# Optimization experiments

Hardware: AMD Instinct MI355X
Metric: run time of the kernel (lower is better)

Reference implementation:

```python
import jax, jax.numpy as jnp
import numpy as np

HIDDEN = 1024
HEADS = 16
HEAD_DIM = HIDDEN // HEADS
LN_EPS = 1e-6


def setup_inputs() -> dict:
    key = jax.random.key(0)
    ks = jax.random.split(key, 12)
    B, S, H = 2, 2048, HIDDEN
    s = 1.0 / np.sqrt(H)
    inp = {
        "hidden_states": jax.random.normal(ks[0], (B, S, H), dtype=jnp.float32),
        "attention_mask": jnp.ones((B, S), dtype=jnp.int32),
        "Wq": jax.random.normal(ks[1], (H, H), dtype=jnp.float32) * s,
        "bq": jax.random.normal(ks[2], (H,), dtype=jnp.float32) * 0.02,
        "Wk": jax.random.normal(ks[3], (H, H), dtype=jnp.float32) * s,
        "bk": jax.random.normal(ks[4], (H,), dtype=jnp.float32) * 0.02,
        "Wv": jax.random.normal(ks[5], (H, H), dtype=jnp.float32) * s,
        "bv": jax.random.normal(ks[6], (H,), dtype=jnp.float32) * 0.02,
        "Wo": jax.random.normal(ks[7], (H, H), dtype=jnp.float32) * s,
        "bo": jax.random.normal(ks[8], (H,), dtype=jnp.float32) * 0.02,
        "ln_g": jnp.ones((H,), dtype=jnp.float32),
        "ln_b": jnp.zeros((H,), dtype=jnp.float32),
    }
    return inp


def _split_heads(x):
    B, S, H = x.shape
    return x.reshape(B, S, HEADS, HEAD_DIM).transpose(0, 2, 1, 3)  # [B,h,S,d]


def reference(hidden_states, attention_mask, Wq, bq, Wk, bk, Wv, bv, Wo, bo, ln_g, ln_b):
    # torch nn.Linear: y = x @ W.T + b
    q = _split_heads(hidden_states @ Wq.T + bq)
    k = _split_heads(hidden_states @ Wk.T + bk)
    v = _split_heads(hidden_states @ Wv.T + bv)

    scores = jnp.einsum("bhqd,bhkd->bhqk", q, k) / np.sqrt(HEAD_DIM)
    # 2D mask path: [B,K] -> [B,1,1,K]; (1-mask)*-1e18 additive bias
    bias = (1.0 - attention_mask[:, None, None, :].astype(scores.dtype)) * -1e18
    probs = jax.nn.softmax(scores + bias, axis=-1)
    # dropout is identity in eval mode
    ctx = jnp.einsum("bhqk,bhkd->bhqd", probs, v)
    B, h, S, d = ctx.shape
    ctx = ctx.transpose(0, 2, 1, 3).reshape(B, S, h * d)

    out = ctx @ Wo.T + bo
    res = out + hidden_states
    mu = jnp.mean(res, axis=-1, keepdims=True)
    var = jnp.mean(jnp.square(res - mu), axis=-1, keepdims=True)
    return (res - mu) * jax.lax.rsqrt(var + LN_EPS) * ln_g + ln_b
```

## Files before the change

kernel.cpp:

```cpp
#include <hip/hip_runtime.h>
#include <hip/hip_bf16.h>

#define SEQ     2048
#define BATCH   2
#define HID     1024
#define NHEADS  16
#define HD      64
#define MTOT    4096
#define LNEPS   1e-6f
#define L2E     1.4426950408889634f
#define SHIFT2  26.0f

typedef __bf16 bf16_t;
typedef bf16_t bf16x8 __attribute__((ext_vector_type(8)));
typedef bf16_t bf16x4 __attribute__((ext_vector_type(4)));
typedef short  short4v __attribute__((ext_vector_type(4)));
typedef float  floatx4 __attribute__((ext_vector_type(4)));

__device__ __forceinline__ floatx4 mfma16(bf16x8 a, bf16x8 b, floatx4 c) {
    return __builtin_amdgcn_mfma_f32_16x16x32_bf16(a, b, c, 0, 0, 0);
}
__device__ __forceinline__ floatx4 mfma16k16(bf16x4 a, bf16x4 b, floatx4 c) {
    short4v as = __builtin_bit_cast(short4v, a);
    short4v bs = __builtin_bit_cast(short4v, b);
    return __builtin_amdgcn_mfma_f32_16x16x16bf16_1k(as, bs, c, 0, 0, 0);
}
__device__ __forceinline__ bf16x8 ldg8(const bf16_t* p) { return *(const bf16x8*)p; }

__device__ __forceinline__ void stage128x32(const bf16_t* __restrict__ g, int row_stride,
                                            int k0, bf16_t* lds, int wave, int lane)
{
#pragma unroll
    for (int j = 0; j < 2; j++) {
        const int rbase = wave * 32 + j * 16;
        const bf16_t* src = g + (size_t)(rbase + (lane >> 2)) * row_stride + k0 + (lane & 3) * 8;
        bf16_t* dst = lds + rbase * 32;
        __builtin_amdgcn_global_load_lds(
            (const __attribute__((address_space(1))) unsigned int*)src,
            (__attribute__((address_space(3))) unsigned int*)dst, 16, 0, 0);
    }
}
__device__ __forceinline__ void stage64x32(const bf16_t* __restrict__ g, int row_stride,
                                           int k0, bf16_t* lds, int wave, int lane)
{
    const int rbase = wave * 16;
    const bf16_t* src = g + (size_t)(rbase + (lane >> 2)) * row_stride + k0 + (lane & 3) * 8;
    bf16_t* dst = lds + rbase * 32;
    __builtin_amdgcn_global_load_lds(
        (const __attribute__((address_space(1))) unsigned int*)src,
        (__attribute__((address_space(3))) unsigned int*)dst, 16, 0, 0);
}

__global__ __launch_bounds__(256) void cvt_kernel(
    const float* sX, const float* sWq, const float* sWk, const float* sWv, const float* sWo,
    bf16_t* dX, bf16_t* dWq, bf16_t* dWk, bf16_t* dWv, bf16_t* dWo)
{
    const int z = blockIdx.z;
    const float* src; bf16_t* dst; int n;
    switch (z) {
        case 0:  src = sX;  dst = dX;  n = MTOT * HID; break;
        case 1:  src = sWq; dst = dWq; n = HID * HID;  break;
        case 2:  src = sWk; dst = dWk; n = HID * HID;  break;
        case 3:  src = sWv; dst = dWv; n = HID * HID;  break;
        default: src = sWo; dst = dWo; n = HID * HID;  break;
    }
    const int n4 = n >> 2;
    const int stride = gridDim.x * blockDim.x;
    for (int i = blockIdx.x * blockDim.x + threadIdx.x; i < n4; i += stride) {
        const float4 v = ((const float4*)src)[i];
        bf16_t o[4] = {(bf16_t)v.x, (bf16_t)v.y, (bf16_t)v.z, (bf16_t)v.w};
        *(unsigned long long*)(dst + 4 * i) = *(unsigned long long*)o;
    }
}

__global__ __launch_bounds__(256) void qkv_kernel(
    const bf16_t* __restrict__ X,
    const bf16_t* __restrict__ Wq, const float* __restrict__ bq,
    const bf16_t* __restrict__ Wk, const float* __restrict__ bk,
    const bf16_t* __restrict__ Wv, const float* __restrict__ bv,
    bf16_t* __restrict__ Qo, bf16_t* __restrict__ Ko, bf16_t* __restrict__ Vo)
{
    const int z = blockIdx.z;
    const bf16_t* W    = (z == 0) ? Wq : (z == 1) ? Wk : Wv;
    const float*  bias = (z == 0) ? bq : (z == 1) ? bk : bv;
    bf16_t*       out  = (z == 0) ? Qo : (z == 1) ? Ko : Vo;

    const int tid  = threadIdx.x;
    const int lane = tid & 63;
    const int wave = tid >> 6;
    const int l16  = lane & 15;
    const int quad = lane >> 4;
    const int m_blk = blockIdx.y * 128;
    const int n_blk = blockIdx.x * 128;
    const int m_w = (wave >> 1) * 64;
    const int n_w = (wave & 1) * 64;

    __shared__ __align__(16) char smem[18432];
    bf16_t* As = (bf16_t*)smem;
    bf16_t* Bs = (bf16_t*)(smem + 8192);

    floatx4 acc[4][4];
#pragma unroll
    for (int i = 0; i < 4; i++)
#pragma unroll
        for (int j = 0; j < 4; j++) acc[i][j] = (floatx4)0.0f;

    for (int k0 = 0; k0 < HID; k0 += 32) {
        __syncthreads();
        stage128x32(X + (size_t)m_blk * HID, HID, k0, As, wave, lane);
        stage128x32(W + (size_t)n_blk * HID, HID, k0, Bs, wave, lane);
        __syncthreads();

        bf16x8 a[4], b[4];
#pragma unroll
        for (int i = 0; i < 4; i++) a[i] = *(const bf16x8*)&As[(m_w + i * 16 + l16) * 32 + quad * 8];
#pragma unroll
        for (int j = 0; j < 4; j++) b[j] = *(const bf16x8*)&Bs[(n_w + j * 16 + l16) * 32 + quad * 8];
#pragma unroll
        for (int i = 0; i < 4; i++)
#pragma unroll
            for (int j = 0; j < 4; j++) acc[i][j] = mfma16(a[i], b[j], acc[i][j]);
    }
    __syncthreads();

    float bv_[4];
#pragma unroll
    for (int j = 0; j < 4; j++) bv_[j] = bias[n_blk + n_w + j * 16 + l16];

    bf16_t* Tw = (bf16_t*)(smem + wave * 4608);

    if (z != 2) {
        const float scale = (z == 0) ? 0.125f : 1.0f;
        const int hN = (n_blk + n_w) >> 6;
#pragma unroll
        for (int ih = 0; ih < 2; ih++) {
#pragma unroll
            for (int i2 = 0; i2 < 2; i2++) {
                const int i = ih * 2 + i2;
#pragma unroll
                for (int j = 0; j < 4; j++)
#pragma unroll
                    for (int r = 0; r < 4; r++)
                        Tw[(i2 * 16 + quad * 4 + r) * 72 + j * 16 + l16] =
                            (bf16_t)((acc[i][j][r] + bv_[j]) * scale);
            }
#pragma unroll
            for (int p = 0; p < 4; p++) {
                const int srow = p * 8 + (lane >> 3);
                const int col  = (lane & 7) * 8;
                bf16x8 v = *(const bf16x8*)&Tw[srow * 72 + col];
                const int m = m_blk + m_w + ih * 32 + srow;
                const int bb = m >> 11, s = m & (SEQ - 1);
                *(bf16x8*)&out[(((size_t)(bb * NHEADS + hN)) * SEQ + s) * HD + col] = v;
            }
        }
    } else {
        const int m0 = m_blk + m_w;
        const int bb = m0 >> 11, s0 = m0 & (SEQ - 1);
#pragma unroll
        for (int jh = 0; jh < 2; jh++) {
#pragma unroll
            for (int j2 = 0; j2 < 2; j2++) {
                const int j = jh * 2 + j2;
#pragma unroll
                for (int i = 0; i < 4; i++) {
                    bf16x4 pk;
#pragma unroll
                    for (int r = 0; r < 4; r++) pk[r] = (bf16_t)(acc[i][j][r] + bv_[j]);
                    *(bf16x4*)&Tw[(j2 * 16 + l16) * 72 + i * 16 + quad * 4] = pk;
                }
            }
#pragma unroll
            for (int p = 0; p < 4; p++) {
                const int srow = p * 8 + (lane >> 3);
                const int col  = (lane & 7) * 8;
                bf16x8 v = *(const bf16x8*)&Tw[srow * 72 + col];
                const int n = n_blk + n_w + jh * 32 + srow;
                const int h = n >> 6, d = n & 63;
                *(bf16x8*)&out[(((size_t)(bb * NHEADS + h)) * HD + d) * SEQ + s0 + col] = v;
            }
        }
    }
}

__global__ __launch_bounds__(256) void attn_kernel(
    const bf16_t* __restrict__ Q, const bf16_t* __restrict__ K,
    const bf16_t* __restrict__ Vt, const int* __restrict__ mask,
    bf16_t* __restrict__ ctx)
{
    const int B   = blockIdx.x;
    const int xcd = B & 7;
    const int idx = B >> 3;
    const int bh  = xcd * 4 + (idx & 3);
    const int q0  = (idx >> 2) * 128;
    const int b   = bh >> 4;
    const int h   = bh & 15;
    const int tid  = threadIdx.x;
    const int wave = tid >> 6;
    const int lane = tid & 63;
    const int l16  = lane & 15;
    const int quad = lane >> 4;
    const int r7   = l16 & 7;

    const bf16_t* Qh = Q  + (size_t)bh * SEQ * HD;
    const bf16_t* Kh = K  + (size_t)bh * SEQ * HD;
    const bf16_t* Vh = Vt + (size_t)bh * HD * SEQ;
    const int*    mk = mask + b * SEQ;

    __shared__ __align__(16) char smem[24576];
    bf16_t* Ks    = (bf16_t*)smem;
    bf16_t* Vs    = (bf16_t*)(smem + 8192);
    float*  bias2 = (float*)(smem + 16384);

    for (int i = tid; i < SEQ; i += 256)
        bias2[i] = (mk[i] ? 0.0f : -1.0e30f) - SHIFT2;

    const int qw = q0 + wave * 32;

    bf16x8 bQ[2][2];
#pragma unroll
    for (int qh = 0; qh < 2; qh++)
#pragma unroll
        for (int kc = 0; kc < 2; kc++)
            bQ[qh][kc] = ldg8(Qh + (size_t)(qw + qh * 16 + l16) * HD + kc * 32 + quad * 8);

    floatx4 O[2][4];
    floatx4 psum[2];
#pragma unroll
    for (int qh = 0; qh < 2; qh++) {
        psum[qh] = (floatx4)0.0f;
#pragma unroll
        for (int dt = 0; dt < 4; dt++) O[qh][dt] = (floatx4)0.0f;
    }

    const int r0 = tid >> 3;
    const int cK = tid & 7;
    const int c0 = cK * 8;
    const int wofsK = r0 * 128 + ((cK ^ (r0 & 7)) << 4);
    const int vr  = r0 & 15;
    const int vg0 = (((cK << 1)    ) ^ vr) << 3;
    const int vg1 = (((cK << 1) + 1) ^ vr) << 3;
    const int kb0 = l16 * 128 + (((quad    ) ^ r7) << 4);
    const int kb1 = l16 * 128 + (((4 + quad) ^ r7) << 4);
    const int vbase = l16 * 128;

    bf16x8 k0v = ldg8(Kh + (size_t)(r0)      * HD + c0);
    bf16x8 k1v = ldg8(Kh + (size_t)(32 + r0) * HD + c0);
    bf16x8 v0v = ldg8(Vh + (size_t)(r0)      * SEQ + c0);
    bf16x8 v1v = ldg8(Vh + (size_t)(32 + r0) * SEQ + c0);

    for (int kt = 0; kt < SEQ; kt += 64) {
        __syncthreads();
        *(bf16x8*)((char*)Ks + wofsK)        = k0v;
        *(bf16x8*)((char*)Ks + wofsK + 4096) = k1v;
        {
            char* vrow = (char*)Vs + r0 * 128;
            bf16x4 lo0 = __builtin_shufflevector(v0v, v0v, 0, 1, 2, 3);
            bf16x4 hi0 = __builtin_shufflevector(v0v, v0v, 4, 5, 6, 7);
            bf16x4 lo1 = __builtin_shufflevector(v1v, v1v, 0, 1, 2, 3);
            bf16x4 hi1 = __builtin_shufflevector(v1v, v1v, 4, 5, 6, 7);
            *(bf16x4*)(vrow + vg0)        = lo0;
            *(bf16x4*)(vrow + vg1)        = hi0;
            *(bf16x4*)(vrow + 4096 + vg0) = lo1;
            *(bf16x4*)(vrow + 4096 + vg1) = hi1;
        }
        __syncthreads();

        if (kt + 64 < SEQ) {
            k0v = ldg8(Kh + (size_t)(kt + 64 + r0) * HD + c0);
            k1v = ldg8(Kh + (size_t)(kt + 96 + r0) * HD + c0);
            v0v = ldg8(Vh + (size_t)(r0)      * SEQ + kt + 64 + c0);
            v1v = ldg8(Vh + (size_t)(32 + r0) * SEQ + kt + 64 + c0);
        }

#pragma unroll
        for (int kvt = 0; kvt < 4; kvt++) {
            bf16x8 aK0 = *(const bf16x8*)((char*)Ks + kb0 + kvt * 2048);
            bf16x8 aK1 = *(const bf16x8*)((char*)Ks + kb1 + kvt * 2048);
            const floatx4 ad = *(const floatx4*)&bias2[kt + kvt * 16 + quad * 4];
            bf16x4 pb[2];
#pragma unroll
            for (int qh = 0; qh < 2; qh++) {
                floatx4 s = (floatx4)0.0f;
                s = mfma16(aK0, bQ[qh][0], s);
                s = mfma16(aK1, bQ[qh][1], s);
                floatx4 p;
#pragma unroll
                for (int r = 0; r < 4; r++)
                    p[r] = __builtin_amdgcn_exp2f(fmaf(s[r], L2E, ad[r]));
                psum[qh] += p;
#pragma unroll
                for (int r = 0; r < 4; r++) pb[qh][r] = (bf16_t)p[r];
            }
            const int vofs = vbase + ((((kvt << 2) + quad) ^ l16) << 3);
#pragma unroll
            for (int dt = 0; dt < 4; dt++) {
                bf16x4 aV = *(const bf16x4*)((char*)Vs + vofs + dt * 2048);
                O[0][dt] = mfma16k16(aV, pb[0], O[0][dt]);
                O[1][dt] = mfma16k16(aV, pb[1], O[1][dt]);
            }
        }
    }

    __syncthreads();

#pragma unroll
    for (int qh = 0; qh < 2; qh++) {
        float su = psum[qh][0] + psum[qh][1] + psum[qh][2] + psum[qh][3];
        su += __shfl_xor(su, 16, 64);
        su += __shfl_xor(su, 32, 64);
        const float linv = (su > 0.0f) ? 1.0f / su : 0.0f;

        bf16_t* Pw = (bf16_t*)(smem + wave * 4608 + qh * 2304);
#pragma unroll
        for (int dt = 0; dt < 4; dt++) {
            floatx4 o = O[qh][dt] * linv;
            bf16x4 pk;
#pragma unroll
            for (int r = 0; r < 4; r++) pk[r] = (bf16_t)o[r];
            *(bf16x4*)&Pw[l16 * 72 + dt * 16 + quad * 4] = pk;
        }
#pragma unroll
        for (int ch = 0; ch < 2; ch++) {
            const int cc  = ch * 64 + lane;
            const int row = cc >> 3;
            const int col = (cc & 7) * 8;
            bf16x8 vv = *(const bf16x8*)&Pw[row * 72 + col];
            *(bf16x8*)&ctx[((size_t)(b * SEQ + qw + qh * 16 + row)) * HID + h * 64 + col] = vv;
        }
    }
}

__global__ __launch_bounds__(256) void oproj_kernel(
    const bf16_t* __restrict__ C, const bf16_t* __restrict__ Wo,
    const float* __restrict__ bo, float* __restrict__ res)
{
    const int tid  = threadIdx.x;
    const int lane = tid & 63;
    const int wave = tid >> 6;
    const int l16  = lane & 15;
    const int quad = lane >> 4;
    const int m_blk = blockIdx.y * 64;
    const int n_blk = blockIdx.x * 128;
    const int n_w   = wave * 32;

    __shared__ __align__(16) char smem[12288];
    bf16_t* As = (bf16_t*)smem;
    bf16_t* Bs = (bf16_t*)(smem + 4096);

    floatx4 acc[4][2];
#pragma unroll
    for (int i = 0; i < 4; i++)
#pragma unroll
        for (int j = 0; j < 2; j++) acc[i][j] = (floatx4)0.0f;

    for (int k0 = 0; k0 < HID; k0 += 32) {
        __syncthreads();
        stage64x32 (C  + (size_t)m_blk * HID, HID, k0, As, wave, lane);
        stage128x32(Wo + (size_t)n_blk * HID, HID, k0, Bs, wave, lane);
        __syncthreads();

        bf16x8 a[4], b[2];
#pragma unroll
        for (int i = 0; i < 4; i++) a[i] = *(const bf16x8*)&As[(i * 16 + l16) * 32 + quad * 8];
#pragma unroll
        for (int j = 0; j < 2; j++) b[j] = *(const bf16x8*)&Bs[(n_w + j * 16 + l16) * 32 + quad * 8];
#pragma unroll
        for (int i = 0; i < 4; i++)
#pragma unroll
            for (int j = 0; j < 2; j++) acc[i][j] = mfma16(a[i], b[j], acc[i][j]);
    }
    __syncthreads();

    float bv_[2];
#pragma unroll
    for (int j = 0; j < 2; j++) bv_[j] = bo[n_blk + n_w + j * 16 + l16];

    float* Tw = (float*)(smem + wave * 2304);
#pragma unroll
    for (int ch = 0; ch < 4; ch++) {
#pragma unroll
        for (int j = 0; j < 2; j++)
#pragma unroll
            for (int r = 0; r < 4; r++)
                Tw[(quad * 4 + r) * 36 + j * 16 + l16] = acc[ch][j][r] + bv_[j];
#pragma unroll
        for (int cc = 0; cc < 2; cc++) {
            const int idx = cc * 64 + lane;
            const int row = idx >> 3;
            const int col = (idx & 7) * 4;
            float4 v = *(const float4*)&Tw[row * 36 + col];
            const int m = m_blk + ch * 16 + row;
            *(float4*)&res[(size_t)m * HID + n_blk + n_w + col] = v;
        }
    }
}

__global__ __launch_bounds__(256) void ln_kernel(
    const float* __restrict__ res, const float* __restrict__ X,
    const float* __restrict__ g, const float* __restrict__ be,
    float* __restrict__ out)
{
    __shared__ float red1[4], red2[4];
    const int row  = blockIdx.x;
    const int lane = threadIdx.x & 63;
    const int wave = threadIdx.x >> 6;
    const float4 a = ((const float4*)(res + (size_t)row * HID))[threadIdx.x];
    const float4 x = ((const float4*)(X   + (size_t)row * HID))[threadIdx.x];
    float4 v;
    v.x = a.x + x.x; v.y = a.y + x.y; v.z = a.z + x.z; v.w = a.w + x.w;

    float s = v.x + v.y + v.z + v.w;
#pragma unroll
    for (int off = 1; off < 64; off <<= 1) s += __shfl_xor(s, off, 64);
    if (lane == 0) red1[wave] = s;
    __syncthreads();
    const float mu = (red1[0] + red1[1] + red1[2] + red1[3]) * (1.0f / HID);

    const float d0 = v.x - mu, d1 = v.y - mu, d2 = v.z - mu, d3 = v.w - mu;
    float ss = d0 * d0 + d1 * d1 + d2 * d2 + d3 * d3;
#pragma unroll
    for (int off = 1; off < 64; off <<= 1) ss += __shfl_xor(ss, off, 64);
    if (lane == 0) red2[wave] = ss;
    __syncthreads();
    const float var = (red2[0] + red2[1] + red2[2] + red2[3]) * (1.0f / HID);
    const float rstd = rsqrtf(var + LNEPS);

    const float4 gv = ((const float4*)g)[threadIdx.x];
    const float4 bv = ((const float4*)be)[threadIdx.x];
    float4 o;
    o.x = d0 * rstd * gv.x + bv.x;
    o.y = d1 * rstd * gv.y + bv.y;
    o.z = d2 * rstd * gv.z + bv.z;
    o.w = d3 * rstd * gv.w + bv.w;
    ((float4*)(out + (size_t)row * HID))[threadIdx.x] = o;
}

extern "C" void kernel_launch(void* const* d_in, const int* in_sizes, int n_in,
                              void* d_out, int out_size, void* d_ws, size_t ws_size,
                              hipStream_t stream)
{
    const float* X  = (const float*)d_in[0];
    const int* mask = (const int*)d_in[1];
    const float* Wq = (const float*)d_in[2];  const float* bq = (const float*)d_in[3];
    const float* Wk = (const float*)d_in[4];  const float* bk = (const float*)d_in[5];
    const float* Wv = (const float*)d_in[6];  const float* bv = (const float*)d_in[7];
    const float* Wo = (const float*)d_in[8];  const float* bo = (const float*)d_in[9];
    const float* g  = (const float*)d_in[10]; const float* be = (const float*)d_in[11];
    float* out = (float*)d_out;

    char* ws = (char*)d_ws;
    bf16_t* Qb  = (bf16_t*)(ws);
    bf16_t* Kb  = (bf16_t*)(ws + (8ull  << 20));
    bf16_t* Vb  = (bf16_t*)(ws + (16ull << 20));
    bf16_t* Cb  = (bf16_t*)(ws + (24ull << 20));
    float*  Rb  = (float*)(ws);
    bf16_t* Xc  = (bf16_t*)(ws + (32ull << 20));
    bf16_t* Wqc = (bf16_t*)(ws + (40ull << 20));
    bf16_t* Wkc = (bf16_t*)(ws + (42ull << 20));
    bf16_t* Wvc = (bf16_t*)(ws + (44ull << 20));
    bf16_t* Woc = (bf16_t*)(ws + (46ull << 20));

    cvt_kernel <<<dim3(128, 1, 5), 256, 0, stream>>>(X, Wq, Wk, Wv, Wo, Xc, Wqc, Wkc, Wvc, Woc);
    qkv_kernel <<<dim3(8, 32, 3), 256, 0, stream>>>(Xc, Wqc, bq, Wkc, bk, Wvc, bv, Qb, Kb, Vb);
    attn_kernel<<<dim3(512), 256, 0, stream>>>(Qb, Kb, Vb, mask, Cb);
    oproj_kernel<<<dim3(8, 64), 256, 0, stream>>>(Cb, Woc, bo, Rb);
    ln_kernel  <<<MTOT, 256, 0, stream>>>(Rb, X, g, be, out);
}
```

Before: 134.7 us.

## Split attention KV sequence across two wave groups and merge partials in LDS

The attention block grows from 256 to 512 threads. Two groups of four waves each process half of the key/value sequence into separate LDS buffers, then the second group writes its partial O and row sums to shared memory and the first group adds them before normalising. The aim is twice as many waves per query tile, hiding latency and shortening each block's serial KV loop. The cost is more LDS per block (40KB), an extra merge barrier, and half the threads idle during the epilogue. The fixed-shift softmax lets the partials be summed without rescaling.

```diff
diff --git a/kernel.cpp b/kernel.cpp
--- a/kernel.cpp
+++ b/kernel.cpp
@@ -7,6 +7,7 @@
 #define NHEADS  16
 #define HD      64
 #define MTOT    4096
+#define KVHALF  1024
 #define LNEPS   1e-6f
 #define L2E     1.4426950408889634f
 #define SHIFT2  26.0f
@@ -183,7 +184,7 @@
     }
 }
 
-__global__ __launch_bounds__(256) void attn_kernel(
+__global__ __launch_bounds__(512, 4) void attn_kernel(
     const bf16_t* __restrict__ Q, const bf16_t* __restrict__ K,
     const bf16_t* __restrict__ Vt, const int* __restrict__ mask,
     bf16_t* __restrict__ ctx)
@@ -197,6 +198,8 @@
     const int h   = bh & 15;
     const int tid  = threadIdx.x;
     const int wave = tid >> 6;
+    const int wq   = wave & 3;
+    const int kh   = wave >> 2;
     const int lane = tid & 63;
     const int l16  = lane & 15;
     const int quad = lane >> 4;
@@ -207,15 +210,16 @@
     const bf16_t* Vh = Vt + (size_t)bh * HD * SEQ;
     const int*    mk = mask + b * SEQ;
 
-    __shared__ __align__(16) char smem[24576];
-    bf16_t* Ks    = (bf16_t*)smem;
-    bf16_t* Vs    = (bf16_t*)(smem + 8192);
-    float*  bias2 = (float*)(smem + 16384);
-
-    for (int i = tid; i < SEQ; i += 256)
+    __shared__ __align__(16) char smem[40960];
+    bf16_t* Ks    = (bf16_t*)(smem + kh * 16384);
+    bf16_t* Vs    = (bf16_t*)(smem + kh * 16384 + 8192);
+    float*  bias2 = (float*)(smem + 32768);
+
+    for (int i = tid; i < SEQ; i += 512)
         bias2[i] = (mk[i] ? 0.0f : -1.0e30f) - SHIFT2;
 
-    const int qw = q0 + wave * 32;
+    const int qw  = q0 + wq * 32;
+    const int kvb = kh * KVHALF;
 
     bf16x8 bQ[2][2];
 #pragma unroll
@@ -233,8 +237,9 @@
         for (int dt = 0; dt < 4; dt++) O[qh][dt] = (floatx4)0.0f;
     }
 
-    const int r0 = tid >> 3;
-    const int cK = tid & 7;
+    const int lt = tid & 255;
+    const int r0 = lt >> 3;
+    const int cK = lt & 7;
     const int c0 = cK * 8;
     const int wofsK = r0 * 128 + ((cK ^ (r0 & 7)) << 4);
     const int vr  = r0 & 15;
@@ -244,12 +249,12 @@
     const int kb1 = l16 * 128 + (((4 + quad) ^ r7) << 4);
     const int vbase = l16 * 128;
 
-    bf16x8 k0v = ldg8(Kh + (size_t)(r0)      * HD + c0);
-    bf16x8 k1v = ldg8(Kh + (size_t)(32 + r0) * HD + c0);
-    bf16x8 v0v = ldg8(Vh + (size_t)(r0)      * SEQ + c0);
-    bf16x8 v1v = ldg8(Vh + (size_t)(32 + r0) * SEQ + c0);
-
-    for (int kt = 0; kt < SEQ; kt += 64) {
+    bf16x8 k0v = ldg8(Kh + (size_t)(kvb + r0)      * HD + c0);
+    bf16x8 k1v = ldg8(Kh + (size_t)(kvb + 32 + r0) * HD + c0);
+    bf16x8 v0v = ldg8(Vh + (size_t)(r0)      * SEQ + kvb + c0);
+    bf16x8 v1v = ldg8(Vh + (size_t)(32 + r0) * SEQ + kvb + c0);
+
+    for (int kt = 0; kt < KVHALF; kt += 64) {
         __syncthreads();
         *(bf16x8*)((char*)Ks + wofsK)        = k0v;
         *(bf16x8*)((char*)Ks + wofsK + 4096) = k1v;
@@ -266,18 +271,18 @@
         }
         __syncthreads();
 
-        if (kt + 64 < SEQ) {
-            k0v = ldg8(Kh + (size_t)(kt + 64 + r0) * HD + c0);
-            k1v = ldg8(Kh + (size_t)(kt + 96 + r0) * HD + c0);
-            v0v = ldg8(Vh + (size_t)(r0)      * SEQ + kt + 64 + c0);
-            v1v = ldg8(Vh + (size_t)(32 + r0) * SEQ + kt + 64 + c0);
+        if (kt + 64 < KVHALF) {
+            k0v = ldg8(Kh + (size_t)(kvb + kt + 64 + r0) * HD + c0);
+            k1v = ldg8(Kh + (size_t)(kvb + kt + 96 + r0) * HD + c0);
+            v0v = ldg8(Vh + (size_t)(r0)      * SEQ + kvb + kt + 64 + c0);
+            v1v = ldg8(Vh + (size_t)(32 + r0) * SEQ + kvb + kt + 64 + c0);
         }
 
 #pragma unroll
         for (int kvt = 0; kvt < 4; kvt++) {
             bf16x8 aK0 = *(const bf16x8*)((char*)Ks + kb0 + kvt * 2048);
             bf16x8 aK1 = *(const bf16x8*)((char*)Ks + kb1 + kvt * 2048);
-            const floatx4 ad = *(const floatx4*)&bias2[kt + kvt * 16 + quad * 4];
+            const floatx4 ad = *(const floatx4*)&bias2[kvb + kt + kvt * 16 + quad * 4];
             bf16x4 pb[2];
 #pragma unroll
             for (int qh = 0; qh < 2; qh++) {
@@ -304,6 +309,30 @@
 
     __syncthreads();
 
+    if (kh == 1) {
+        float* mw = (float*)(smem + wq * 10240) + lane * 40;
+#pragma unroll
+        for (int qh = 0; qh < 2; qh++) {
+#pragma unroll
+            for (int dt = 0; dt < 4; dt++)
+                *(floatx4*)(mw + qh * 16 + dt * 4) = O[qh][dt];
+            *(floatx4*)(mw + 32 + qh * 4) = psum[qh];
+        }
+    }
+    __syncthreads();
+    if (kh == 1) return;
+
+    {
+        const float* mr = (const float*)(smem + wq * 10240) + lane * 40;
+#pragma unroll
+        for (int qh = 0; qh < 2; qh++) {
+#pragma unroll
+            for (int dt = 0; dt < 4; dt++)
+                O[qh][dt] += *(const floatx4*)(mr + qh * 16 + dt * 4);
+            psum[qh] += *(const floatx4*)(mr + 32 + qh * 4);
+        }
+    }
+
 #pragma unroll
     for (int qh = 0; qh < 2; qh++) {
         float su = psum[qh][0] + psum[qh][1] + psum[qh][2] + psum[qh][3];
@@ -311,7 +340,7 @@
         su += __shfl_xor(su, 32, 64);
         const float linv = (su > 0.0f) ? 1.0f / su : 0.0f;
 
-        bf16_t* Pw = (bf16_t*)(smem + wave * 4608 + qh * 2304);
+        bf16_t* Pw = (bf16_t*)(smem + wq * 10240 + qh * 2304);
 #pragma unroll
         for (int dt = 0; dt < 4; dt++) {
             floatx4 o = O[qh][dt] * linv;
@@ -463,7 +492,7 @@
 
     cvt_kernel <<<dim3(128, 1, 5), 256, 0, stream>>>(X, Wq, Wk, Wv, Wo, Xc, Wqc, Wkc, Wvc, Woc);
     qkv_kernel <<<dim3(8, 32, 3), 256, 0, stream>>>(Xc, Wqc, bq, Wkc, bk, Wvc, bv, Qb, Kb, Vb);
-    attn_kernel<<<dim3(512), 256, 0, stream>>>(Qb, Kb, Vb, mask, Cb);
+    attn_kernel<<<dim3(512), 512, 0, stream>>>(Qb, Kb, Vb, mask, Cb);
     oproj_kernel<<<dim3(8, 64), 256, 0, stream>>>(Cb, Woc, bo, Rb);
     ln_kernel  <<<MTOT, 256, 0, stream>>>(Rb, X, g, be, out);
 }
```

Measured after the change: 131.3 us. -2.5%, faster.
